# Kernel optimization log

Hardware: AMD Instinct MI355X
Metric: run time of the kernel (lower is better)

The kernel has to match this reference:

```python
import jax, jax.numpy as jnp
import numpy as np

B, N, A = 8, 8192, 10   # batch, points, attributes (xyz + normal + 4 extra)
G, M = 512, 32          # num_group, group_size
EPS = 1e-5


def setup_inputs() -> dict:
    key = jax.random.key(0)
    ks = jax.random.split(key, 16)
    w = lambda k, s: jax.random.normal(k, s, jnp.float32) * 0.02
    inp = {"xyz": jax.random.normal(ks[0], (B, N, A), jnp.float32)}
    # Light_T_Net params (conv1 6->64, conv2 64->512, fc 512->36)
    inp["tn_w1"], inp["tn_b1"] = w(ks[1], (64, 6)), jnp.zeros(64, jnp.float32)
    inp["tn_g1"], inp["tn_be1"] = jnp.ones(64, jnp.float32), jnp.zeros(64, jnp.float32)
    inp["tn_w2"], inp["tn_b2"] = w(ks[2], (512, 64)), jnp.zeros(512, jnp.float32)
    inp["tn_g2"], inp["tn_be2"] = jnp.ones(512, jnp.float32), jnp.zeros(512, jnp.float32)
    inp["tn_fw"], inp["tn_fb"] = w(ks[3], (36, 512)), jnp.zeros(36, jnp.float32)
    # Light_PointNet_Encoder convs: A->128->256->512->1024
    for i, (co, ci) in enumerate([(128, A), (256, 128), (512, 256), (1024, 512)], 1):
        inp[f"w{i}"], inp[f"b{i}"] = w(ks[3 + i], (co, ci)), jnp.zeros(co, jnp.float32)
        inp[f"g{i}"], inp[f"be{i}"] = jnp.ones(co, jnp.float32), jnp.zeros(co, jnp.float32)
    return inp


def _bn(x, g, b):
    # training-mode BatchNorm1d: stats over (batch, length) for [BG, n, C]
    m = x.mean((0, 1))
    v = x.var((0, 1))
    return (x - m) * jax.lax.rsqrt(v + EPS) * g + b


def _fps(xyz, npoint):
    # sequential farthest-point sampling (deterministic start index 0)
    coords = xyz[:, :, :3]
    b, n, _ = xyz.shape

    def step(carry, _):
        dist, far = carry
        cen = jnp.take_along_axis(xyz, far[:, None, None], axis=1)  # [B,1,A]
        d = jnp.sum((coords - cen[:, :, :3]) ** 2, -1)              # [B,N]
        dist = jnp.minimum(dist, d)
        return (dist, jnp.argmax(dist, -1)), (far, cen[:, 0, :])

    dist0 = jnp.full((b, n), 1e10, xyz.dtype)
    far0 = jnp.zeros((b,), jnp.int32)
    _, (idx, attrs) = jax.lax.scan(step, (dist0, far0), None, length=npoint)
    return idx.T, attrs.transpose(1, 0, 2)  # [B,G], [B,G,A]


def _forward(xyz, tn_w1, tn_b1, tn_g1, tn_be1, tn_w2, tn_b2, tn_g2, tn_be2,
             tn_fw, tn_fb, w1, b1, g1, be1, w2, b2, g2, be2,
             w3, b3, g3, be3, w4, b4, g4, be4):
    b = xyz.shape[0]
    # ---- Group_for_all_attribute ----
    _, cen = _fps(xyz, G)                                           # [B,G,A]
    # cdist over full attribute dim; squared distance gives identical topk order
    d2 = (jnp.sum(cen ** 2, -1)[:, :, None] + jnp.sum(xyz ** 2, -1)[:, None, :]
          - 2.0 * jnp.einsum('bga,bna->bgn', cen, xyz))             # [B,G,N]
    idx = jax.lax.top_k(-d2, M)[1]                                  # [B,G,M] smallest dists
    nb = xyz[jnp.arange(b)[:, None, None], idx]                     # [B,G,M,A]
    nb = jnp.concatenate([nb[..., :3] - cen[:, :, None, :3], nb[..., 3:]], -1)
    # ---- Light_PointNet_Encoder ----
    pg = nb.reshape(b * G, M, A)
    x6 = pg[:, :, :6]
    # Light_T_Net
    h = jax.nn.relu(_bn(x6 @ tn_w1.T + tn_b1, tn_g1, tn_be1))
    h = jax.nn.relu(_bn(h @ tn_w2.T + tn_b2, tn_g2, tn_be2))
    t = (h.max(1) @ tn_fw.T + tn_fb + jnp.eye(6, dtype=xyz.dtype).reshape(36)).reshape(-1, 6, 6)
    pg = jnp.concatenate([jnp.einsum('bnc,bcd->bnd', x6, t), pg[:, :, 6:]], -1)
    # 1x1 conv stack (= per-point linear) with training-mode BN
    h = jax.nn.relu(_bn(pg @ w1.T + b1, g1, be1))
    h = jax.nn.relu(_bn(h @ w2.T + b2, g2, be2))
    h = jax.nn.relu(_bn(h @ w3.T + b3, g3, be3))
    h = _bn(h @ w4.T + b4, g4, be4)
    return h.max(1).reshape(b, G, -1)                               # [B,G,1024]


def reference(xyz, tn_w1, tn_b1, tn_g1, tn_be1, tn_w2, tn_b2, tn_g2, tn_be2,
              tn_fw, tn_fb, w1, b1, g1, be1, w2, b2, g2, be2,
              w3, b3, g3, be3, w4, b4, g4, be4):
    return _forward(xyz, tn_w1, tn_b1, tn_g1, tn_be1, tn_w2, tn_b2, tn_g2, tn_be2,
                    tn_fw, tn_fb, w1, b1, g1, be1, w2, b2, g2, be2,
                    w3, b3, g3, be3, w4, b4, g4, be4)
```

## Files before the change

### kernel.cpp

```cpp
#include <hip/hip_runtime.h>
#include <hip/hip_bf16.h>

static constexpr int B_  = 8;
static constexpr int N_  = 8192;
static constexpr int A_  = 10;
static constexpr int G_  = 512;
static constexpr int M_  = 32;
static constexpr int S_TOT = B_ * G_ * M_;
static constexpr float EPS_ = 1e-5f;
static constexpr float FMAXV = 3.402823466e+38f;

__device__ __forceinline__ float b2f(__hip_bfloat16 h) { return __bfloat162float(h); }
__device__ __forceinline__ unsigned short f2bs(float f) {
    __hip_bfloat16 h = __float2bfloat16(f);
    return *reinterpret_cast<unsigned short*>(&h);
}

typedef __bf16 bf16x8 __attribute__((ext_vector_type(8)));
typedef float  f32x4  __attribute__((ext_vector_type(4)));

__device__ __forceinline__ unsigned fkey(float f) {
    unsigned u = __float_as_uint(f);
    return u ^ ((unsigned)((int)u >> 31) | 0x80000000u);
}

template<int CTRL, bool MAXOP>
__device__ __forceinline__ unsigned long long dpp_step(unsigned long long k) {
    const int lo = (int)(unsigned)k;
    const int hi = (int)(unsigned)(k >> 32);
    const int lo2 = __builtin_amdgcn_update_dpp(lo, lo, CTRL, 0xf, 0xf, false);
    const int hi2 = __builtin_amdgcn_update_dpp(hi, hi, CTRL, 0xf, 0xf, false);
    const unsigned long long o =
        ((unsigned long long)(unsigned)hi2 << 32) | (unsigned)lo2;
    if (MAXOP) return (o > k) ? o : k;
    else       return (o < k) ? o : k;
}
template<bool MAXOP>
__device__ __forceinline__ unsigned long long dpp_reduce(unsigned long long k) {
    k = dpp_step<0x111, MAXOP>(k);
    k = dpp_step<0x112, MAXOP>(k);
    k = dpp_step<0x114, MAXOP>(k);
    k = dpp_step<0x118, MAXOP>(k);
    k = dpp_step<0x142, MAXOP>(k);
    k = dpp_step<0x143, MAXOP>(k);
    return k;
}

template<int CTRL, int RMASK>
__device__ __forceinline__ float dpp_fadd(float v) {
    const int o = __builtin_amdgcn_update_dpp(0, __float_as_int(v), CTRL, RMASK, 0xf, true);
    return v + __int_as_float(o);
}
__device__ __forceinline__ float dpp_wave_sum(float v) {
    v = dpp_fadd<0x111, 0xf>(v);
    v = dpp_fadd<0x112, 0xf>(v);
    v = dpp_fadd<0x114, 0xf>(v);
    v = dpp_fadd<0x118, 0xf>(v);
    v = dpp_fadd<0x142, 0xa>(v);
    v = dpp_fadd<0x143, 0xc>(v);
    return v;
}

static constexpr size_t CO_XYZ  = 0;
static constexpr size_t CO_TNW1 = 655360, CO_TNB1 = 655744, CO_TNG1 = 655808, CO_TNBE1 = 655872;
static constexpr size_t CO_TNW2 = 655936, CO_TNB2 = 688704, CO_TNG2 = 689216, CO_TNBE2 = 689728;
static constexpr size_t CO_TNFW = 690240, CO_TNFB = 708672;
static constexpr size_t CO_W1 = 708708, CO_B1 = 709988, CO_G1 = 710116, CO_BE1 = 710244;
static constexpr size_t CO_W2 = 710372, CO_B2 = 743140, CO_G2 = 743396, CO_BE2 = 743652;
static constexpr size_t CO_W3 = 743908, CO_B3 = 874980, CO_G3 = 875492, CO_BE3 = 876004;
static constexpr size_t CO_W4 = 876516, CO_B4 = 1400804, CO_G4 = 1401828, CO_BE4 = 1402852;
static constexpr size_t CO_TOT = 1403876;

static constexpr size_t WB_TNW2 = 0;
static constexpr size_t WB_W2   = 32768;
static constexpr size_t WB_W3   = 65536;
static constexpr size_t WB_W4   = 196608;
static constexpr size_t WB_TOT  = 720896;

#define MB_ (1024ull * 1024ull)
static constexpr size_t OFF_CANON = 0;
static constexpr size_t OFF_CEN   = 6 * MB_;
static constexpr size_t OFF_XSQ   = 6 * MB_ + 256 * 1024;
static constexpr size_t OFF_STATS = 6 * MB_ + 512 * 1024;
static constexpr size_t OFF_COEFF = 6 * MB_ + 576 * 1024;
static constexpr size_t OFF_DUMMY = 6 * MB_ + 640 * 1024;
static constexpr size_t OFF_TMAT  = 6 * MB_ + 768 * 1024;
static constexpr size_t OFF_WBF16 = 8 * MB_;
static constexpr size_t OFF_PG    = 10 * MB_;
static constexpr size_t OFF_TZ1   = 16 * MB_;
static constexpr size_t OFF_TPMAX = 32 * MB_;
static constexpr size_t OFF_TPMIN = 40 * MB_;
static constexpr size_t OFF_Z1    = 16 * MB_;
static constexpr size_t OFF_MM4X  = 16 * MB_;
static constexpr size_t OFF_MM4N  = 32 * MB_;
static constexpr size_t OFF_Z2    = 48 * MB_;
static constexpr size_t OFF_Z3    = 112 * MB_;
static constexpr size_t NEED_A = 240 * MB_;
static constexpr int NCHUNK_ = 8;
static constexpr int CSAMP_  = S_TOT / NCHUNK_;

static constexpr int STF_T1 = 0;
static constexpr int STF_T2 = 128;
static constexpr int STF_M1 = 1152;
static constexpr int STF_M2 = 1408;
static constexpr int STF_M3 = 1920;
static constexpr int STF_M4 = 2944;

struct Ptrs { const void* p[27]; };

__global__ __launch_bounds__(256)
void convert_kernel(Ptrs ptrs, float* __restrict__ canon, float* __restrict__ stats)
{
    const size_t gid = (size_t)blockIdx.x * 256 + threadIdx.x;
    if (gid < 5120) stats[gid] = 0.f;
    if (gid >= CO_TOT) return;
    constexpr size_t offs[28] = {0, 655360, 655744, 655808, 655872, 655936,
        688704, 689216, 689728, 690240, 708672, 708708, 709988, 710116, 710244,
        710372, 743140, 743396, 743652, 743908, 874980, 875492, 876004, 876516,
        1400804, 1401828, 1402852, 1403876};
    int j = 0;
    while (j < 26 && gid >= offs[j + 1]) ++j;
    const size_t loc = gid - offs[j];
    const bool fp32m = (((const unsigned short*)ptrs.p[3])[0] == 0);
    float v;
    if (fp32m) v = ((const float*)ptrs.p[j])[loc];
    else       v = b2f(((const __hip_bfloat16*)ptrs.p[j])[loc]);
    canon[gid] = v;
}

__global__ __launch_bounds__(256)
void wconv_kernel(const float* __restrict__ canon, __hip_bfloat16* __restrict__ wb)
{
    const size_t gid = (size_t)blockIdx.x * 256 + threadIdx.x;
    if (gid >= WB_TOT) return;
    constexpr size_t offs[5] = {0, 32768, 65536, 196608, 720896};
    constexpr size_t co[4]   = {CO_TNW2, CO_W2, CO_W3, CO_W4};
    int j = 0;
    while (j < 3 && gid >= offs[j + 1]) ++j;
    wb[gid] = __float2bfloat16(canon[co[j] + (gid - offs[j])]);
}

__global__ __launch_bounds__(256)
void fps_kernel(const float* __restrict__ xyz, float* __restrict__ cen)
{
    __shared__ float lx[N_], ly[N_], lz[N_];
    __shared__ unsigned long long red[2][4];
    __shared__ int fidx[G_];

    const int t = threadIdx.x;
    const int b = blockIdx.x;
    const float* xb = xyz + (size_t)b * N_ * A_;

    float px[32], py[32], pz[32], dist[32];
#pragma unroll
    for (int j = 0; j < 32; ++j) {
        const int i = j * 256 + t;
        px[j] = xb[(size_t)i * A_ + 0];
        py[j] = xb[(size_t)i * A_ + 1];
        pz[j] = xb[(size_t)i * A_ + 2];
        lx[i] = px[j]; ly[i] = py[j]; lz[i] = pz[j];
        dist[j] = 1e10f;
    }
    __syncthreads();

    int far = 0;
    for (int it = 0; it < G_; ++it) {
        if (t == 0) fidx[it] = far;
        const float cx = lx[far], cy = ly[far], cz = lz[far];

        float bv = -1.f; int bi = 0;
#pragma unroll
        for (int j = 0; j < 32; ++j) {
            const float dx = px[j] - cx, dy = py[j] - cy, dz = pz[j] - cz;
            const float d = dx * dx + dy * dy + dz * dz;
            const float nd = fminf(dist[j], d);
            dist[j] = nd;
            if (nd > bv) { bv = nd; bi = j * 256 + t; }
        }
        unsigned long long best =
            ((unsigned long long)__float_as_uint(bv) << 32) | (unsigned)~(unsigned)bi;
        best = dpp_reduce<true>(best);
        const int p = it & 1;
        if ((t & 63) == 63) red[p][t >> 6] = best;
        __syncthreads();
        unsigned long long m = red[p][0];
#pragma unroll
        for (int w = 1; w < 4; ++w) {
            const unsigned long long o = red[p][w];
            m = (o > m) ? o : m;
        }
        far = (int)(~(unsigned)m) & (N_ - 1);
    }
    __syncthreads();
    for (int e = t; e < G_ * A_; e += 256) {
        const int it = e / A_;
        const int a  = e - it * A_;
        cen[((size_t)b * G_ + it) * A_ + a] = xb[(size_t)fidx[it] * A_ + a];
    }
}

__global__ __launch_bounds__(256)
void xsq_kernel(const float* __restrict__ xyz, float* __restrict__ xsq)
{
    const int i = blockIdx.x * 256 + threadIdx.x;
    float s = 0.f;
#pragma unroll
    for (int a = 0; a < A_; ++a) { const float v = xyz[(size_t)i * A_ + a]; s += v * v; }
    xsq[i] = s;
}

__global__ __launch_bounds__(256)
void knn_kernel(const float* __restrict__ xyz, const float* __restrict__ cen,
                const float* __restrict__ xsq, float* __restrict__ pg)
{
    __shared__ float ca[A_];
    __shared__ unsigned long long red[2][4];
    __shared__ int win[M_];

    const int t  = threadIdx.x;
    const int bg = blockIdx.x;
    const int b  = bg >> 9;
    const float* xb  = xyz + (size_t)b * N_ * A_;
    const float* xsb = xsq + (size_t)b * N_;

    if (t < A_) ca[t] = cen[(size_t)bg * A_ + t];
    __syncthreads();
    float csq = 0.f;
#pragma unroll
    for (int a = 0; a < A_; ++a) csq += ca[a] * ca[a];

    float d2r[32];
    float bv = FMAXV; int bi = 0;
#pragma unroll
    for (int j = 0; j < 32; ++j) {
        const int i = j * 256 + t;
        float dot = 0.f;
#pragma unroll
        for (int a = 0; a < A_; ++a) dot += xb[(size_t)i * A_ + a] * ca[a];
        const float v = (csq + xsb[i]) - 2.f * dot;
        d2r[j] = v;
        if (v < bv) { bv = v; bi = i; }
    }

    for (int it = 0; it < M_; ++it) {
        unsigned long long key =
            ((unsigned long long)fkey(bv) << 32) | (unsigned)bi;
        key = dpp_reduce<false>(key);
        const int p = it & 1;
        if ((t & 63) == 63) red[p][t >> 6] = key;
        __syncthreads();
        unsigned long long m = red[p][0];
#pragma unroll
        for (int w = 1; w < 4; ++w) {
            const unsigned long long o = red[p][w];
            m = (o < m) ? o : m;
        }
        const int wi = (int)((unsigned)m) & (N_ - 1);
        if (t == (wi & 255)) {
            win[it] = wi;
            const int wj = wi >> 8;
#pragma unroll
            for (int j = 0; j < 32; ++j) if (j == wj) d2r[j] = FMAXV;
            bv = FMAXV; bi = 0;
#pragma unroll
            for (int j = 0; j < 32; ++j) {
                const float v = d2r[j];
                if (v < bv) { bv = v; bi = j * 256 + t; }
            }
        }
    }
    __syncthreads();
    if (t < M_) {
        const int i = win[t];
        for (int a = 0; a < A_; ++a) {
            float v = xb[(size_t)i * A_ + a];
            if (a < 3) v -= ca[a];
            pg[((size_t)bg * M_ + t) * A_ + a] = v;
        }
    }
}

template<int K, int C>
__global__ __launch_bounds__(256)
void mlp_small_kernel(const float* __restrict__ pgx,
                      const float* __restrict__ W,
                      const float* __restrict__ Bv,
                      __hip_bfloat16* __restrict__ Zout,
                      float* __restrict__ stats)
{
    __shared__ float w[C * K];
    __shared__ float bb[C];
    __shared__ float lstat[C][2];
    const int t = threadIdx.x;
    for (int i = t; i < C * K; i += 256) w[i] = W[i];
    for (int i = t; i < C; i += 256) bb[i] = Bv[i];
    for (int i = t; i < 2 * C; i += 256) ((float*)lstat)[i] = 0.f;
    __syncthreads();

    const size_t s = (size_t)blockIdx.x * 256 + t;
    float x[K];
#pragma unroll
    for (int k = 0; k < K; ++k) x[k] = pgx[s * A_ + k];

    ushort4 u;
    for (int c = 0; c < C; ++c) {
        float z = bb[c];
#pragma unroll
        for (int k = 0; k < K; ++k) z += w[c * K + k] * x[k];
        const unsigned short zs = f2bs(z);
        const int cm = c & 3;
        if (cm == 0) u.x = zs; else if (cm == 1) u.y = zs; else if (cm == 2) u.z = zs;
        else { u.w = zs; *reinterpret_cast<ushort4*>(Zout + s * C + (c - 3)) = u; }

        const float sv = dpp_wave_sum(z);
        const float sq = dpp_wave_sum(z * z);
        if ((t & 63) == 63) { atomicAdd(&lstat[c][0], sv); atomicAdd(&lstat[c][1], sq); }
    }
    __syncthreads();
    for (int c = t; c < C; c += 256) {
        atomicAdd(&stats[c],     lstat[c][0]);
        atomicAdd(&stats[C + c], lstat[c][1]);
    }
}

__global__ __launch_bounds__(256)
void finalize_kernel(const float* __restrict__ stats, const float* __restrict__ g,
                     const float* __restrict__ be, float* __restrict__ coeff, int C)
{
    for (int c = threadIdx.x; c < C; c += 256) {
        const float mean = stats[c] * (1.f / (float)S_TOT);
        const float var  = stats[C + c] * (1.f / (float)S_TOT) - mean * mean;
        const float sc = g[c] * rsqrtf(fmaxf(var, 0.f) + EPS_);
        coeff[c]     = sc;
        coeff[C + c] = be[c] - mean * sc;
    }
}

template<int K, int N, bool POOL>
__global__ __launch_bounds__(256)
void gemm_mfma_kernel(const __hip_bfloat16* __restrict__ Zin,
                      const float* __restrict__ coeff,
                      const __hip_bfloat16* __restrict__ Wb,
                      const float* __restrict__ Bv,
                      __hip_bfloat16* __restrict__ Zout,
                      float* __restrict__ maxbuf,
                      float* __restrict__ minbuf,
                      float* __restrict__ stats)
{
    constexpr int PITCH = 72;
    constexpr int NX = N / 128;
    __shared__ __hip_bfloat16 As[128 * PITCH];
    __shared__ __hip_bfloat16 Bs[128 * PITCH];
    __shared__ float csc[K];
    __shared__ float csh[K];
    __shared__ float lstat[256];

    const int t    = threadIdx.x;
    const int lane = t & 63;
    const int wave = t >> 6;
    const int wm   = wave >> 1;
    const int wn   = wave & 1;
    const int ln   = lane & 15;
    const int quad = lane >> 4;
    const int bid = blockIdx.x;
    const int xcd = bid & 7;
    const int i   = bid >> 3;
    const int bx  = i % NX;
    const int by  = (i / NX) * 8 + xcd;
    const int c0  = bx * 128;
    const int s0  = by * 128;

    for (int ii = t; ii < K; ii += 256) { csc[ii] = coeff[ii]; csh[ii] = coeff[K + ii]; }
    lstat[t] = 0.f;

    f32x4 acc[4][4];
#pragma unroll
    for (int ni = 0; ni < 4; ++ni) {
        const float bj = Bv[c0 + wn * 64 + ni * 16 + ln];
#pragma unroll
        for (int mi = 0; mi < 4; ++mi) acc[mi][ni] = (f32x4){bj, bj, bj, bj};
    }

    for (int kt = 0; kt < K; kt += 64) {
        __syncthreads();
#pragma unroll
        for (int p = 0; p < 4; ++p) {
            const int id = p * 256 + t;
            const int r  = id >> 3;
            const int sg = id & 7;
            const float4 raw = *reinterpret_cast<const float4*>(
                Zin + (size_t)(s0 + r) * K + kt + sg * 8);
            const __hip_bfloat162* p2 = reinterpret_cast<const __hip_bfloat162*>(&raw);
            unsigned short tmp[8] __attribute__((aligned(16)));
#pragma unroll
            for (int j = 0; j < 4; ++j) {
                const int k0 = kt + sg * 8 + 2 * j;
                const float x0 = fmaxf(b2f(p2[j].x) * csc[k0]     + csh[k0],     0.f);
                const float x1 = fmaxf(b2f(p2[j].y) * csc[k0 + 1] + csh[k0 + 1], 0.f);
                tmp[2 * j]     = f2bs(x0);
                tmp[2 * j + 1] = f2bs(x1);
            }
            *reinterpret_cast<float4*>(&As[r * PITCH + sg * 8]) =
                *reinterpret_cast<const float4*>(tmp);
            *reinterpret_cast<float4*>(&Bs[r * PITCH + sg * 8]) =
                *reinterpret_cast<const float4*>(Wb + (size_t)(c0 + r) * K + kt + sg * 8);
        }
        __syncthreads();

        bf16x8 af[4][2], bf_[4][2];
#pragma unroll
        for (int mi = 0; mi < 4; ++mi)
#pragma unroll
            for (int kk = 0; kk < 2; ++kk)
                af[mi][kk] = *reinterpret_cast<const bf16x8*>(
                    &As[(wm * 64 + mi * 16 + ln) * PITCH + quad * 8 + kk * 32]);
#pragma unroll
        for (int ni = 0; ni < 4; ++ni)
#pragma unroll
            for (int kk = 0; kk < 2; ++kk)
                bf_[ni][kk] = *reinterpret_cast<const bf16x8*>(
                    &Bs[(wn * 64 + ni * 16 + ln) * PITCH + quad * 8 + kk * 32]);
#pragma unroll
        for (int kk = 0; kk < 2; ++kk)
#pragma unroll
            for (int mi = 0; mi < 4; ++mi)
#pragma unroll
                for (int ni = 0; ni < 4; ++ni)
                    acc[mi][ni] = __builtin_amdgcn_mfma_f32_16x16x32_bf16(
                        af[mi][kk], bf_[ni][kk], acc[mi][ni], 0, 0, 0);
    }

#pragma unroll
    for (int ni = 0; ni < 4; ++ni) {
        float sv = 0.f, sq = 0.f;
#pragma unroll
        for (int mi = 0; mi < 4; ++mi)
#pragma unroll
            for (int r = 0; r < 4; ++r) {
                const float v = acc[mi][ni][r];
                sv += v; sq += v * v;
            }
        sv += __shfl_xor(sv, 16); sq += __shfl_xor(sq, 16);
        sv += __shfl_xor(sv, 32); sq += __shfl_xor(sq, 32);
        if (quad == 0) {
            const int col = wn * 64 + ni * 16 + ln;
            atomicAdd(&lstat[col], sv);
            atomicAdd(&lstat[128 + col], sq);
        }
    }
    __syncthreads();
    if (t < 128) {
        atomicAdd(&stats[c0 + t],     lstat[t]);
        atomicAdd(&stats[N + c0 + t], lstat[128 + t]);
    }

    if constexpr (POOL) {
#pragma unroll
        for (int ni = 0; ni < 4; ++ni) {
            float mx0 = -FMAXV, mn0 = FMAXV, mx1 = -FMAXV, mn1 = FMAXV;
#pragma unroll
            for (int mi = 0; mi < 2; ++mi)
#pragma unroll
                for (int r = 0; r < 4; ++r) {
                    const float v = acc[mi][ni][r];
                    mx0 = fmaxf(mx0, v); mn0 = fminf(mn0, v);
                }
#pragma unroll
            for (int mi = 2; mi < 4; ++mi)
#pragma unroll
                for (int r = 0; r < 4; ++r) {
                    const float v = acc[mi][ni][r];
                    mx1 = fmaxf(mx1, v); mn1 = fminf(mn1, v);
                }
            mx0 = fmaxf(mx0, __shfl_xor(mx0, 16)); mn0 = fminf(mn0, __shfl_xor(mn0, 16));
            mx0 = fmaxf(mx0, __shfl_xor(mx0, 32)); mn0 = fminf(mn0, __shfl_xor(mn0, 32));
            mx1 = fmaxf(mx1, __shfl_xor(mx1, 16)); mn1 = fminf(mn1, __shfl_xor(mn1, 16));
            mx1 = fmaxf(mx1, __shfl_xor(mx1, 32)); mn1 = fminf(mn1, __shfl_xor(mn1, 32));
            if (quad == 0) {
                const int col = c0 + wn * 64 + ni * 16 + ln;
                const int g   = (s0 >> 5) + wm * 2;
                maxbuf[(size_t)g * N + col]       = mx0;
                minbuf[(size_t)g * N + col]       = mn0;
                maxbuf[(size_t)(g + 1) * N + col] = mx1;
                minbuf[(size_t)(g + 1) * N + col] = mn1;
            }
        }
    } else {
#pragma unroll
        for (int mi = 0; mi < 4; ++mi)
#pragma unroll
            for (int r = 0; r < 4; ++r) {
                const size_t row = (size_t)(s0 + wm * 64 + mi * 16 + quad * 4 + r);
#pragma unroll
                for (int ni = 0; ni < 4; ++ni) {
                    const int col = c0 + wn * 64 + ni * 16 + ln;
                    Zout[row * N + col] = __float2bfloat16(acc[mi][ni][r]);
                }
            }
    }
}

__global__ __launch_bounds__(64)
void tnet_fc_kernel(const float* __restrict__ maxbuf, const float* __restrict__ minbuf,
                    const float* __restrict__ coeff, const float* __restrict__ FW,
                    const float* __restrict__ FB, float* __restrict__ tmat)
{
    __shared__ float h[512];
    const int bg = blockIdx.x;
    const int t  = threadIdx.x;
    for (int i = t; i < 512; i += 64) {
        const float sc = coeff[i], sh = coeff[512 + i];
        const float v = (sc >= 0.f) ? maxbuf[(size_t)bg * 512 + i] : minbuf[(size_t)bg * 512 + i];
        h[i] = fmaxf(sc * v + sh, 0.f);
    }
    __syncthreads();
    if (t < 36) {
        float acc = FB[t] + ((t % 7 == 0) ? 1.f : 0.f);
        for (int k = 0; k < 512; ++k) acc += FW[t * 512 + k] * h[k];
        tmat[(size_t)bg * 36 + t] = acc;
    }
}

__global__ __launch_bounds__(256)
void transform_kernel(float* __restrict__ pg, const float* __restrict__ tmat)
{
    const size_t s = (size_t)blockIdx.x * 256 + threadIdx.x;
    const int bg = (int)(s >> 5);
    float x[6];
#pragma unroll
    for (int c = 0; c < 6; ++c) x[c] = pg[s * A_ + c];
    const float* tm = tmat + (size_t)bg * 36;
#pragma unroll
    for (int d = 0; d < 6; ++d) {
        float o = 0.f;
#pragma unroll
        for (int c = 0; c < 6; ++c) o += x[c] * tm[c * 6 + d];
        pg[s * A_ + d] = o;
    }
}

__global__ __launch_bounds__(256)
void output_kernel(const float* __restrict__ maxbuf, const float* __restrict__ minbuf,
                   const float* __restrict__ coeff, const unsigned short* __restrict__ probe,
                   void* __restrict__ out)
{
    const size_t e = (size_t)blockIdx.x * 256 + threadIdx.x;
    const int c = (int)(e & 1023);
    const float sc = coeff[c], sh = coeff[1024 + c];
    const float v = (sc >= 0.f) ? maxbuf[e] : minbuf[e];
    const float r = sc * v + sh;
    if (probe[0] == 0) ((float*)out)[e] = r;
    else ((__hip_bfloat16*)out)[e] = __float2bfloat16(r);
}

extern "C" void kernel_launch(void* const* d_in, const int* in_sizes, int n_in,
                              void* d_out, int out_size, void* d_ws, size_t ws_size,
                              hipStream_t stream)
{
    char* ws = (char*)d_ws;
    float*          canon = (float*)(ws + OFF_CANON);
    float*          cen   = (float*)(ws + OFF_CEN);
    float*          xsq   = (float*)(ws + OFF_XSQ);
    float*          stats = (float*)(ws + OFF_STATS);
    float*          coeff = (float*)(ws + OFF_COEFF);
    float*          dummy = (float*)(ws + OFF_DUMMY);
    float*          tmat  = (float*)(ws + OFF_TMAT);
    __hip_bfloat16* wbf   = (__hip_bfloat16*)(ws + OFF_WBF16);
    float*          tpmax = (float*)(ws + OFF_TPMAX);
    float*          tpmin = (float*)(ws + OFF_TPMIN);
    float*          pg    = (float*)(ws + OFF_PG);
    __hip_bfloat16* tz1   = (__hip_bfloat16*)(ws + OFF_TZ1);
    __hip_bfloat16* z1    = (__hip_bfloat16*)(ws + OFF_Z1);
    __hip_bfloat16* z2    = (__hip_bfloat16*)(ws + OFF_Z2);
    __hip_bfloat16* z3    = (__hip_bfloat16*)(ws + OFF_Z3);
    float*          mmax4 = (float*)(ws + OFF_MM4X);
    float*          mmin4 = (float*)(ws + OFF_MM4N);

    Ptrs ptrs;
    for (int i = 0; i < 27; ++i) ptrs.p[i] = d_in[i];

    const float* cxyz = canon + CO_XYZ;

    convert_kernel<<<(int)((CO_TOT + 255) / 256), 256, 0, stream>>>(ptrs, canon, stats);
    wconv_kernel<<<(int)((WB_TOT + 255) / 256), 256, 0, stream>>>(canon, wbf);

    fps_kernel<<<B_, 256, 0, stream>>>(cxyz, cen);
    xsq_kernel<<<(B_ * N_) / 256, 256, 0, stream>>>(cxyz, xsq);
    knn_kernel<<<B_ * G_, 256, 0, stream>>>(cxyz, cen, xsq, pg);

    mlp_small_kernel<6, 64><<<S_TOT / 256, 256, 0, stream>>>(
        pg, canon + CO_TNW1, canon + CO_TNB1, tz1, stats + STF_T1);
    finalize_kernel<<<1, 256, 0, stream>>>(stats + STF_T1, canon + CO_TNG1, canon + CO_TNBE1,
                                           coeff + STF_T1, 64);
    gemm_mfma_kernel<64, 512, true><<<4 * (S_TOT / 128), 256, 0, stream>>>(
        tz1, coeff + STF_T1, wbf + WB_TNW2, canon + CO_TNB2, nullptr, tpmax, tpmin, stats + STF_T2);
    finalize_kernel<<<1, 256, 0, stream>>>(stats + STF_T2, canon + CO_TNG2, canon + CO_TNBE2,
                                           coeff + STF_T2, 512);
    tnet_fc_kernel<<<B_ * G_, 64, 0, stream>>>(tpmax, tpmin, coeff + STF_T2,
                                               canon + CO_TNFW, canon + CO_TNFB, tmat);
    transform_kernel<<<S_TOT / 256, 256, 0, stream>>>(pg, tmat);

    mlp_small_kernel<10, 128><<<S_TOT / 256, 256, 0, stream>>>(
        pg, canon + CO_W1, canon + CO_B1, z1, stats + STF_M1);
    finalize_kernel<<<1, 256, 0, stream>>>(stats + STF_M1, canon + CO_G1, canon + CO_BE1,
                                           coeff + STF_M1, 128);
    gemm_mfma_kernel<128, 256, false><<<2 * (S_TOT / 128), 256, 0, stream>>>(
        z1, coeff + STF_M1, wbf + WB_W2, canon + CO_B2, z2, nullptr, nullptr, stats + STF_M2);
    finalize_kernel<<<1, 256, 0, stream>>>(stats + STF_M2, canon + CO_G2, canon + CO_BE2,
                                           coeff + STF_M2, 256);

    if (ws_size >= NEED_A) {
        gemm_mfma_kernel<256, 512, false><<<4 * (S_TOT / 128), 256, 0, stream>>>(
            z2, coeff + STF_M2, wbf + WB_W3, canon + CO_B3, z3, nullptr, nullptr, stats + STF_M3);
        finalize_kernel<<<1, 256, 0, stream>>>(stats + STF_M3, canon + CO_G3, canon + CO_BE3,
                                               coeff + STF_M3, 512);
        gemm_mfma_kernel<512, 1024, true><<<8 * (S_TOT / 128), 256, 0, stream>>>(
            z3, coeff + STF_M3, wbf + WB_W4, canon + CO_B4, nullptr, mmax4, mmin4, stats + STF_M4);
    } else {
        for (int c = 0; c < NCHUNK_; ++c) {
            gemm_mfma_kernel<256, 512, false><<<4 * (CSAMP_ / 128), 256, 0, stream>>>(
                z2 + (size_t)c * CSAMP_ * 256, coeff + STF_M2, wbf + WB_W3, canon + CO_B3,
                z3, nullptr, nullptr, stats + STF_M3);
        }
        finalize_kernel<<<1, 256, 0, stream>>>(stats + STF_M3, canon + CO_G3, canon + CO_BE3,
                                               coeff + STF_M3, 512);
        for (int c = 0; c < NCHUNK_; ++c) {
            gemm_mfma_kernel<256, 512, false><<<4 * (CSAMP_ / 128), 256, 0, stream>>>(
                z2 + (size_t)c * CSAMP_ * 256, coeff + STF_M2, wbf + WB_W3, canon + CO_B3,
                z3, nullptr, nullptr, dummy);
            gemm_mfma_kernel<512, 1024, true><<<8 * (CSAMP_ / 128), 256, 0, stream>>>(
                z3, coeff + STF_M3, wbf + WB_W4, canon + CO_B4, nullptr,
                mmax4 + (size_t)(c * CSAMP_ / 32) * 1024,
                mmin4 + (size_t)(c * CSAMP_ / 32) * 1024, stats + STF_M4);
        }
    }
    finalize_kernel<<<1, 256, 0, stream>>>(stats + STF_M4, canon + CO_G4, canon + CO_BE4,
                                           coeff + STF_M4, 1024);

    output_kernel<<<(B_ * G_ * 1024) / 256, 256, 0, stream>>>(
        mmax4, mmin4, coeff + STF_M4, (const unsigned short*)d_in[3], d_out);
}
```

Measured before the change: 1.362 ms.

## Process two batches per FPS block with 512 threads, fetching centroids from global

The FPS kernel now runs 4 blocks of 512 threads, each handling two batch items at once with 16 points per thread per batch. The two independent argmax reductions share a single barrier per iteration, which gives more instruction-level parallelism. The shared-memory coordinate copies are removed and centroid coordinates are read from global memory (L1/L2) instead. This halves the number of blocks, leaving most CUs idle, and adds a global-load latency to each serial iteration in exchange for fewer barrier rounds overall.

```diff
diff --git a/kernel.cpp b/kernel.cpp
--- a/kernel.cpp
+++ b/kernel.cpp
@@ -140,62 +140,88 @@
     wb[gid] = __float2bfloat16(canon[co[j] + (gid - offs[j])]);
 }
 
-__global__ __launch_bounds__(256)
+__global__ __launch_bounds__(512)
 void fps_kernel(const float* __restrict__ xyz, float* __restrict__ cen)
 {
-    __shared__ float lx[N_], ly[N_], lz[N_];
-    __shared__ unsigned long long red[2][4];
-    __shared__ int fidx[G_];
+    __shared__ unsigned long long red[2][2][8];
+    __shared__ int fidx[2][G_];
 
     const int t = threadIdx.x;
-    const int b = blockIdx.x;
-    const float* xb = xyz + (size_t)b * N_ * A_;
-
-    float px[32], py[32], pz[32], dist[32];
-#pragma unroll
-    for (int j = 0; j < 32; ++j) {
-        const int i = j * 256 + t;
-        px[j] = xb[(size_t)i * A_ + 0];
-        py[j] = xb[(size_t)i * A_ + 1];
-        pz[j] = xb[(size_t)i * A_ + 2];
-        lx[i] = px[j]; ly[i] = py[j]; lz[i] = pz[j];
-        dist[j] = 1e10f;
-    }
-    __syncthreads();
-
-    int far = 0;
+    const float* xb0 = xyz + (size_t)(2 * blockIdx.x)     * N_ * A_;
+    const float* xb1 = xyz + (size_t)(2 * blockIdx.x + 1) * N_ * A_;
+
+    float px0[16], py0[16], pz0[16], d0[16];
+    float px1[16], py1[16], pz1[16], d1[16];
+#pragma unroll
+    for (int j = 0; j < 16; ++j) {
+        const int i = j * 512 + t;
+        px0[j] = xb0[(size_t)i * A_ + 0];
+        py0[j] = xb0[(size_t)i * A_ + 1];
+        pz0[j] = xb0[(size_t)i * A_ + 2];
+        px1[j] = xb1[(size_t)i * A_ + 0];
+        py1[j] = xb1[(size_t)i * A_ + 1];
+        pz1[j] = xb1[(size_t)i * A_ + 2];
+        d0[j] = 1e10f; d1[j] = 1e10f;
+    }
+    __syncthreads();
+
+    int far0 = 0, far1 = 0;
     for (int it = 0; it < G_; ++it) {
-        if (t == 0) fidx[it] = far;
-        const float cx = lx[far], cy = ly[far], cz = lz[far];
-
-        float bv = -1.f; int bi = 0;
-#pragma unroll
-        for (int j = 0; j < 32; ++j) {
-            const float dx = px[j] - cx, dy = py[j] - cy, dz = pz[j] - cz;
-            const float d = dx * dx + dy * dy + dz * dz;
-            const float nd = fminf(dist[j], d);
-            dist[j] = nd;
-            if (nd > bv) { bv = nd; bi = j * 256 + t; }
-        }
-        unsigned long long best =
-            ((unsigned long long)__float_as_uint(bv) << 32) | (unsigned)~(unsigned)bi;
-        best = dpp_reduce<true>(best);
+        if (t == 0) fidx[0][it] = far0;
+        if (t == 1) fidx[1][it] = far1;
+        const float2 c0xy = *reinterpret_cast<const float2*>(xb0 + (size_t)far0 * A_);
+        const float2 c1xy = *reinterpret_cast<const float2*>(xb1 + (size_t)far1 * A_);
+        const float  c0z  = xb0[(size_t)far0 * A_ + 2];
+        const float  c1z  = xb1[(size_t)far1 * A_ + 2];
+
+        float bv0 = -1.f, bv1 = -1.f; int bi0 = 0, bi1 = 0;
+#pragma unroll
+        for (int j = 0; j < 16; ++j) {
+            const float ax = px0[j] - c0xy.x, ay = py0[j] - c0xy.y, az = pz0[j] - c0z;
+            const float nd = fminf(d0[j], ax * ax + ay * ay + az * az);
+            d0[j] = nd;
+            if (nd > bv0) { bv0 = nd; bi0 = j * 512 + t; }
+        }
+#pragma unroll
+        for (int j = 0; j < 16; ++j) {
+            const float ax = px1[j] - c1xy.x, ay = py1[j] - c1xy.y, az = pz1[j] - c1z;
+            const float nd = fminf(d1[j], ax * ax + ay * ay + az * az);
+            d1[j] = nd;
+            if (nd > bv1) { bv1 = nd; bi1 = j * 512 + t; }
+        }
+        unsigned long long k0 =
+            ((unsigned long long)__float_as_uint(bv0) << 32) | (unsigned)~(unsigned)bi0;
+        unsigned long long k1 =
+            ((unsigned long long)__float_as_uint(bv1) << 32) | (unsigned)~(unsigned)bi1;
+        k0 = dpp_reduce<true>(k0);
+        k1 = dpp_reduce<true>(k1);
         const int p = it & 1;
-        if ((t & 63) == 63) red[p][t >> 6] = best;
+        if ((t & 63) == 63) {
+            red[p][0][t >> 6] = k0;
+            red[p][1][t >> 6] = k1;
+        }
         __syncthreads();
-        unsigned long long m = red[p][0];
-#pragma unroll
-        for (int w = 1; w < 4; ++w) {
-            const unsigned long long o = red[p][w];
-            m = (o > m) ? o : m;
-        }
-        far = (int)(~(unsigned)m) & (N_ - 1);
-    }
-    __syncthreads();
-    for (int e = t; e < G_ * A_; e += 256) {
-        const int it = e / A_;
-        const int a  = e - it * A_;
-        cen[((size_t)b * G_ + it) * A_ + a] = xb[(size_t)fidx[it] * A_ + a];
+        unsigned long long m0 = red[p][0][0];
+        unsigned long long m1 = red[p][1][0];
+#pragma unroll
+        for (int w = 1; w < 8; ++w) {
+            const unsigned long long o0 = red[p][0][w];
+            m0 = (o0 > m0) ? o0 : m0;
+            const unsigned long long o1 = red[p][1][w];
+            m1 = (o1 > m1) ? o1 : m1;
+        }
+        far0 = (int)(~(unsigned)m0) & (N_ - 1);
+        far1 = (int)(~(unsigned)m1) & (N_ - 1);
+    }
+    __syncthreads();
+    for (int e = t; e < 2 * G_ * A_; e += 512) {
+        const int bb = e / (G_ * A_);
+        const int r  = e - bb * (G_ * A_);
+        const int it = r / A_;
+        const int a  = r - it * A_;
+        const float* x = bb ? xb1 : xb0;
+        cen[((size_t)(2 * blockIdx.x + bb) * G_ + it) * A_ + a] =
+            x[(size_t)fidx[bb][it] * A_ + a];
     }
 }
 
@@ -584,7 +610,7 @@
     convert_kernel<<<(int)((CO_TOT + 255) / 256), 256, 0, stream>>>(ptrs, canon, stats);
     wconv_kernel<<<(int)((WB_TOT + 255) / 256), 256, 0, stream>>>(canon, wbf);
 
-    fps_kernel<<<B_, 256, 0, stream>>>(cxyz, cen);
+    fps_kernel<<<B_ / 2, 512, 0, stream>>>(cxyz, cen);
     xsq_kernel<<<(B_ * N_) / 256, 256, 0, stream>>>(cxyz, xsq);
     knn_kernel<<<B_ * G_, 256, 0, stream>>>(cxyz, cen, xsq, pg);
 
```

Result: slower. 2.005 ms (+47.2%).
